# Performance work log

Measured on AMD Instinct MI355X. Metric: run time of the kernel, lower is better.

## Reference

```python
import jax, jax.numpy as jnp
import numpy as np

E = 768
H = 12
D = E // H  # 64


def setup_inputs() -> dict:
    key = jax.random.key(0)
    ks = jax.random.split(key, 12)
    B, S = 4, 2048
    scale = 1.0 / np.sqrt(E)
    inp = {
        "q": jax.random.normal(ks[0], (B, S, E), jnp.float32),
        "k": jax.random.normal(ks[1], (B, S, E), jnp.float32),
        "v": jax.random.normal(ks[2], (B, S, E), jnp.float32),
        "mask": jax.random.randint(ks[3], (B, S), 0, 2, jnp.int32),
        "Wq": jax.random.normal(ks[4], (E, E), jnp.float32) * scale,
        "bq": jnp.zeros((E,), jnp.float32),
        "Wk": jax.random.normal(ks[5], (E, E), jnp.float32) * scale,
        "bk": jnp.zeros((E,), jnp.float32),
        "Wv": jax.random.normal(ks[6], (E, E), jnp.float32) * scale,
        "bv": jnp.zeros((E,), jnp.float32),
        "Wo": jax.random.normal(ks[7], (E, E), jnp.float32) * scale,
        "bo": jnp.zeros((E,), jnp.float32),
    }
    return inp


def reference(q, k, v, mask, Wq, bq, Wk, bk, Wv, bv, Wo, bo):
    B, Sq, _ = q.shape
    Sk = k.shape[1]
    # QKV projections, split into heads: [B, H, S, D]
    qh = (q @ Wq + bq).reshape(B, Sq, H, D).transpose(0, 2, 1, 3)
    kh = (k @ Wk + bk).reshape(B, Sk, H, D).transpose(0, 2, 1, 3)
    vh = (v @ Wv + bv).reshape(B, Sk, H, D).transpose(0, 2, 1, 3)
    scores = jnp.einsum("bhqd,bhkd->bhqk", qh, kh) / jnp.sqrt(jnp.float32(D))
    # enc=True padding-mask path: positions where mask==0 get -1e9 added
    bias = jnp.where(mask == 0, jnp.float32(-1e9), jnp.float32(0.0))  # [B, Sk]
    scores = scores + bias[:, None, None, :]
    weights = jax.nn.softmax(scores, axis=-1)
    # dropout is identity in eval mode
    ctx = jnp.einsum("bhqk,bhkd->bqhd", weights, vh).reshape(B, Sq, E)
    return ctx @ Wo + bo
```

## Files before the change

kernel.cpp:

```cpp
#include <hip/hip_runtime.h>
#include <hip/hip_bf16.h>
#include <stdint.h>


typedef __bf16 bf16x8 __attribute__((ext_vector_type(8)));
typedef __bf16 bf16x4 __attribute__((ext_vector_type(4)));
typedef float floatx4 __attribute__((ext_vector_type(4)));

#define MFMA_BF16(a, b, c) __builtin_amdgcn_mfma_f32_16x16x32_bf16(a, b, c, 0, 0, 0)


__device__ __forceinline__ void glds16(const __bf16* g, __bf16* l) {
  __builtin_amdgcn_global_load_lds(
      (const __attribute__((address_space(1))) unsigned int*)g,
      (__attribute__((address_space(3))) unsigned int*)l, 16, 0, 0);
}

#if __has_builtin(__builtin_amdgcn_permlane32_swap)
__device__ __forceinline__ void perm32_swap(unsigned int& a, unsigned int& b) {
  auto r = __builtin_amdgcn_permlane32_swap(a, b, false, false);
  a = r[0];
  b = r[1];
}
#else
__device__ __forceinline__ void perm32_swap(unsigned int& a, unsigned int& b) {
  asm("v_permlane32_swap_b32 %0, %1" : "+v"(a), "+v"(b));
}
#endif

#if __has_builtin(__builtin_amdgcn_permlane16_swap)
__device__ __forceinline__ void perm16_swap(unsigned int& a, unsigned int& b) {
  auto r = __builtin_amdgcn_permlane16_swap(a, b, false, false);
  a = r[0];
  b = r[1];
}
#else
__device__ __forceinline__ void perm16_swap(unsigned int& a, unsigned int& b) {
  asm("v_permlane16_swap_b32 %0, %1" : "+v"(a), "+v"(b));
}
#endif

__global__ __launch_bounds__(256) void prep_transpose(
    const float* __restrict__ W0, const float* __restrict__ W1,
    const float* __restrict__ W2, const float* __restrict__ W3,
    __bf16* __restrict__ T0, __bf16* __restrict__ T1,
    __bf16* __restrict__ T2, __bf16* __restrict__ T3,
    const int* __restrict__ mask, float* __restrict__ biasF) {
  const int z = blockIdx.z;
  const float* W = (z == 0) ? W0 : (z == 1) ? W1 : (z == 2) ? W2 : W3;
  __bf16* T = (z == 0) ? T0 : (z == 1) ? T1 : (z == 2) ? T2 : T3;
  __shared__ float t[32][33];
  const int tx = threadIdx.x & 31, ty = threadIdx.x >> 5;
  const int kb = blockIdx.x * 32, nb = blockIdx.y * 32;
#pragma unroll
  for (int j = 0; j < 4; ++j)
    t[ty + j * 8][tx] = W[(size_t)(kb + ty + j * 8) * 768 + nb + tx];
  if (z == 3 && blockIdx.y == 0 && blockIdx.x < 8) {
    const int idx = blockIdx.x * 1024 + threadIdx.x * 4;
    const int4 m4 = *(const int4*)&mask[idx];
    float4 f4;
    f4.x = m4.x ? 0.0f : -1e5f;
    f4.y = m4.y ? 0.0f : -1e5f;
    f4.z = m4.z ? 0.0f : -1e5f;
    f4.w = m4.w ? 0.0f : -1e5f;
    *(float4*)&biasF[idx] = f4;
  }
  __syncthreads();
#pragma unroll
  for (int j = 0; j < 4; ++j)
    T[(size_t)(nb + ty + j * 8) * 768 + kb + tx] = (__bf16)t[tx][ty + j * 8];
}

__global__ __launch_bounds__(256) void qkv_gemm(
    const __bf16* __restrict__ Wtq, const __bf16* __restrict__ Wtk,
    const __bf16* __restrict__ Wtv, const float* __restrict__ Xq,
    const float* __restrict__ Xk, const float* __restrict__ Xv,
    const float* __restrict__ bq, const float* __restrict__ bk,
    const float* __restrict__ bv, __bf16* __restrict__ Qh,
    __bf16* __restrict__ Kh, __bf16* __restrict__ Vt) {
  __shared__ __align__(16) __bf16 As[2][128 * 32];
  __shared__ __align__(16) __bf16 Bs[2][128 * 32];
  const int gid = blockIdx.x + 6 * blockIdx.y + 384 * blockIdx.z;
  const int swz = (gid & 7) * 144 + (gid >> 3);
  const int z = swz / 384;
  const int rem = swz - z * 384;
  const int by = rem / 6;
  const int bx = rem - by * 6;

  const __bf16* Aop = (z == 0) ? Wtq : (z == 1) ? Wtk : Wtv;
  const float* Bop = (z == 0) ? Xq : (z == 1) ? Xk : Xv;
  const float* bias = (z == 0) ? bq : (z == 1) ? bk : bv;
  __bf16* Dst = (z == 0) ? Qh : (z == 1) ? Kh : Vt;
  const int m0 = bx * 128, n0 = by * 128;

  const int tid = threadIdx.x, lane = tid & 63, w = tid >> 6;
  const int quad = lane >> 4, l16 = lane & 15;
  const int wm = (w >> 1) * 64, wn = (w & 1) * 64;

  const int garow = w * 32 + (lane >> 2);
  const int gacol = (lane & 3) * 8;
  const __bf16* gA = Aop + (size_t)(m0 + garow) * 768 + gacol;
  const int brow = tid >> 3, bcol = (tid & 7) * 4;
  const float* gB = Bop + (size_t)(n0 + brow) * 768 + bcol;

  floatx4 acc[4][4] = {};
  float4 f[4];

  glds16(gA, &As[0][w * 1024]);
  glds16(gA + (size_t)16 * 768, &As[0][w * 1024 + 512]);
#pragma unroll
  for (int j = 0; j < 4; ++j) f[j] = *(const float4*)&gB[(size_t)(32 * j) * 768];
#pragma unroll
  for (int j = 0; j < 4; ++j) {
    bf16x4 pv;
    pv[0] = (__bf16)f[j].x; pv[1] = (__bf16)f[j].y;
    pv[2] = (__bf16)f[j].z; pv[3] = (__bf16)f[j].w;
    *(bf16x4*)&Bs[0][(brow + 32 * j) * 32 + bcol] = pv;
  }
#pragma unroll
  for (int j = 0; j < 4; ++j) f[j] = *(const float4*)&gB[(size_t)(32 * j) * 768 + 32];
  __syncthreads();

#pragma unroll 2
  for (int it = 0; it < 24; ++it) {
    const int c = it & 1;
    if (it < 23) {
      glds16(gA + (size_t)(it + 1) * 32, &As[c ^ 1][w * 1024]);
      glds16(gA + (size_t)(it + 1) * 32 + (size_t)16 * 768,
             &As[c ^ 1][w * 1024 + 512]);
    }
    bf16x8 af[4], bfr[4];
#pragma unroll
    for (int t = 0; t < 4; ++t) {
      af[t] = *(const bf16x8*)&As[c][(wm + t * 16 + l16) * 32 + quad * 8];
      bfr[t] = *(const bf16x8*)&Bs[c][(wn + t * 16 + l16) * 32 + quad * 8];
    }
    if (it < 23) {
#pragma unroll
      for (int j = 0; j < 4; ++j) {
        bf16x4 pv;
        pv[0] = (__bf16)f[j].x; pv[1] = (__bf16)f[j].y;
        pv[2] = (__bf16)f[j].z; pv[3] = (__bf16)f[j].w;
        *(bf16x4*)&Bs[c ^ 1][(brow + 32 * j) * 32 + bcol] = pv;
      }
    }
    if (it < 22) {
#pragma unroll
      for (int j = 0; j < 4; ++j)
        f[j] = *(const float4*)&gB[(size_t)(32 * j) * 768 + (it + 2) * 32];
    }
#pragma unroll
    for (int mt = 0; mt < 4; ++mt)
#pragma unroll
      for (int nt = 0; nt < 4; ++nt)
        acc[mt][nt] = MFMA_BF16(af[mt], bfr[nt], acc[mt][nt]);
    __syncthreads();
  }

  const float qs = (z == 0) ? 0.18033688011112042f : 1.0f;
#pragma unroll
  for (int mt = 0; mt < 4; ++mt) {
    const int e = m0 + wm + mt * 16 + quad * 4;
    const float4 b4 = *(const float4*)&bias[e];
    const int h = e >> 6, d = e & 63;
#pragma unroll
    for (int nt = 0; nt < 4; ++nt) {
      const int s = n0 + wn + nt * 16 + l16;
      const int bb = s >> 11, sr = s & 2047;
      const float v0 = (acc[mt][nt][0] + b4.x) * qs;
      const float v1 = (acc[mt][nt][1] + b4.y) * qs;
      const float v2 = (acc[mt][nt][2] + b4.z) * qs;
      const float v3 = (acc[mt][nt][3] + b4.w) * qs;
      if (z < 2) {
        bf16x4 pv;
        pv[0] = (__bf16)v0; pv[1] = (__bf16)v1; pv[2] = (__bf16)v2; pv[3] = (__bf16)v3;
        const int col = (z == 0) ? d : ((((d >> 3) ^ (sr & 7)) << 3) | (d & 7));
        *(bf16x4*)&Dst[((size_t)(bb * 12 + h) * 2048 + sr) * 64 + col] = pv;
      } else {
        const size_t rowbase = ((size_t)(bb * 12 + h) * 64 + d) * 2048;
        const int shi = sr & ~63, sblk = (sr >> 3) & 7, soff = sr & 7;
        Dst[rowbase + 0 * 2048 + shi + (((sblk ^ ((d + 0) & 7))) << 3) + soff] = (__bf16)v0;
        Dst[rowbase + 1 * 2048 + shi + (((sblk ^ ((d + 1) & 7))) << 3) + soff] = (__bf16)v1;
        Dst[rowbase + 2 * 2048 + shi + (((sblk ^ ((d + 2) & 7))) << 3) + soff] = (__bf16)v2;
        Dst[rowbase + 3 * 2048 + shi + (((sblk ^ ((d + 3) & 7))) << 3) + soff] = (__bf16)v3;
      }
    }
  }
}

__global__ __launch_bounds__(256) void out_gemm(const __bf16* __restrict__ Wto,
                                                const __bf16* __restrict__ Ctx,
                                                const float* __restrict__ bo,
                                                float* __restrict__ Out) {
  __shared__ __align__(16) __bf16 As[2][128 * 32];
  __shared__ __align__(16) __bf16 Bs[2][128 * 32];
  const int gid = blockIdx.x + 6 * blockIdx.y;
  const int swz = (gid & 7) * 48 + (gid >> 3);
  const int by = swz / 6;
  const int bx = swz - by * 6;
  const int m0 = bx * 128, n0 = by * 128;
  const int tid = threadIdx.x, lane = tid & 63, w = tid >> 6;
  const int quad = lane >> 4, l16 = lane & 15;
  const int wm = (w >> 1) * 64, wn = (w & 1) * 64;

  const int grow = w * 32 + (lane >> 2);
  const int gcol = (lane & 3) * 8;
  const __bf16* gA = Wto + (size_t)(m0 + grow) * 768 + gcol;
  const __bf16* gB = Ctx + (size_t)(n0 + grow) * 768 + gcol;

  floatx4 acc[4][4] = {};

  glds16(gA, &As[0][w * 1024]);
  glds16(gA + (size_t)16 * 768, &As[0][w * 1024 + 512]);
  glds16(gB, &Bs[0][w * 1024]);
  glds16(gB + (size_t)16 * 768, &Bs[0][w * 1024 + 512]);
  __syncthreads();

#pragma unroll 2
  for (int it = 0; it < 24; ++it) {
    const int c = it & 1;
    if (it < 23) {
      glds16(gA + (size_t)(it + 1) * 32, &As[c ^ 1][w * 1024]);
      glds16(gA + (size_t)(it + 1) * 32 + (size_t)16 * 768,
             &As[c ^ 1][w * 1024 + 512]);
      glds16(gB + (size_t)(it + 1) * 32, &Bs[c ^ 1][w * 1024]);
      glds16(gB + (size_t)(it + 1) * 32 + (size_t)16 * 768,
             &Bs[c ^ 1][w * 1024 + 512]);
    }
    bf16x8 af[4], bfr[4];
#pragma unroll
    for (int t = 0; t < 4; ++t) {
      af[t] = *(const bf16x8*)&As[c][(wm + t * 16 + l16) * 32 + quad * 8];
      bfr[t] = *(const bf16x8*)&Bs[c][(wn + t * 16 + l16) * 32 + quad * 8];
    }
#pragma unroll
    for (int mt = 0; mt < 4; ++mt)
#pragma unroll
      for (int nt = 0; nt < 4; ++nt)
        acc[mt][nt] = MFMA_BF16(af[mt], bfr[nt], acc[mt][nt]);
    __syncthreads();
  }

#pragma unroll
  for (int mt = 0; mt < 4; ++mt) {
    const int e = m0 + wm + mt * 16 + quad * 4;
    const float4 b4 = *(const float4*)&bo[e];
#pragma unroll
    for (int nt = 0; nt < 4; ++nt) {
      const int s = n0 + wn + nt * 16 + l16;
      float4 r;
      r.x = acc[mt][nt][0] + b4.x;
      r.y = acc[mt][nt][1] + b4.y;
      r.z = acc[mt][nt][2] + b4.z;
      r.w = acc[mt][nt][3] + b4.w;
      *(float4*)&Out[(size_t)s * 768 + e] = r;
    }
  }
}

__global__ __launch_bounds__(256) void attn_kernel(
    const __bf16* __restrict__ Qh, const __bf16* __restrict__ Kh,
    const __bf16* __restrict__ Vt, const float* __restrict__ biasF,
    __bf16* __restrict__ ctx) {
  const int lid = blockIdx.x + 16 * blockIdx.y;
  const int swz = (lid & 7) * 96 + (lid >> 3);
  const int qx = swz & 15, bh = swz >> 4;
  const int b = bh / 12, h = bh - b * 12;
  const int tid = threadIdx.x, lane = tid & 63, w = tid >> 6;
  const int quad = lane >> 4, l16 = lane & 15;
  const int q0 = qx * 128 + w * 32;

  __shared__ __align__(16) __bf16 Ks[2][64 * 64];
  __shared__ __align__(16) __bf16 Vs[2][64 * 64];

  const __bf16* Qbase = Qh + (size_t)bh * 2048 * 64;
  const __bf16* Kbase = Kh + (size_t)bh * 2048 * 64;
  const __bf16* Vbase = Vt + (size_t)bh * 64 * 2048;
  const float* biasB = biasF + b * 2048;

  bf16x8 bqf[2][2];
#pragma unroll
  for (int qt = 0; qt < 2; ++qt)
#pragma unroll
    for (int c = 0; c < 2; ++c)
      bqf[qt][c] =
          *(const bf16x8*)&Qbase[(size_t)(q0 + qt * 16 + l16) * 64 + c * 32 + quad * 8];

  const int r0 = (w * 2) * 8 + (lane >> 3);
  const int r1 = (w * 2 + 1) * 8 + (lane >> 3);
  const int scol = (lane & 7) * 8;
  const int d0 = (w * 2) * 512;
  const int d1 = (w * 2 + 1) * 512;
  const int col0 = (quad ^ (l16 & 7)) * 8;

  glds16(&Kbase[(size_t)r0 * 64 + scol], &Ks[0][d0]);
  glds16(&Kbase[(size_t)r1 * 64 + scol], &Ks[0][d1]);
  glds16(&Vbase[(size_t)r0 * 2048 + scol], &Vs[0][d0]);
  glds16(&Vbase[(size_t)r1 * 2048 + scol], &Vs[0][d1]);

  floatx4 o[4][2] = {};
  floatx4 os[2] = {};
  bf16x8 ones8;
#pragma unroll
  for (int j = 0; j < 8; ++j) ones8[j] = (__bf16)1.0f;

  for (int it = 0; it < 32; ++it) {
    const int kt = it * 64;
    const int cur = it & 1;
    const int nxt = cur ^ 1;
    const int nkt = (kt + 64) & 2047;

    __syncthreads();

    glds16(&Kbase[(size_t)(nkt + r0) * 64 + scol], &Ks[nxt][d0]);
    glds16(&Kbase[(size_t)(nkt + r1) * 64 + scol], &Ks[nxt][d1]);
    glds16(&Vbase[(size_t)r0 * 2048 + nkt + scol], &Vs[nxt][d0]);
    glds16(&Vbase[(size_t)r1 * 2048 + nkt + scol], &Vs[nxt][d1]);

    floatx4 sc[4][2];
#pragma unroll
    for (int t = 0; t < 4; ++t) {
      const float4 bf4 = *(const float4*)&biasB[kt + t * 16 + quad * 4];
      bf16x8 ak0 = *(const bf16x8*)&Ks[cur][(t * 16 + l16) * 64 + col0];
      bf16x8 ak1 = *(const bf16x8*)&Ks[cur][(t * 16 + l16) * 64 + (col0 ^ 32)];
#pragma unroll
      for (int qt = 0; qt < 2; ++qt) {
        floatx4 zz;
        zz[0] = bf4.x; zz[1] = bf4.y; zz[2] = bf4.z; zz[3] = bf4.w;
        zz = MFMA_BF16(ak0, bqf[qt][0], zz);
        zz = MFMA_BF16(ak1, bqf[qt][1], zz);
        sc[t][qt] = zz;
      }
    }
    unsigned int u[4][2][2];
#pragma unroll
    for (int t = 0; t < 4; ++t)
#pragma unroll
      for (int qt = 0; qt < 2; ++qt) {
        const float e0 = __builtin_amdgcn_exp2f(sc[t][qt][0]);
        const float e1 = __builtin_amdgcn_exp2f(sc[t][qt][1]);
        const float e2 = __builtin_amdgcn_exp2f(sc[t][qt][2]);
        const float e3 = __builtin_amdgcn_exp2f(sc[t][qt][3]);
        asm("v_cvt_pk_bf16_f32 %0, %1, %2" : "=v"(u[t][qt][0]) : "v"(e0), "v"(e1));
        asm("v_cvt_pk_bf16_f32 %0, %1, %2" : "=v"(u[t][qt][1]) : "v"(e2), "v"(e3));
      }
#pragma unroll
    for (int c = 0; c < 2; ++c) {
      bf16x8 bp[2];
#pragma unroll
      for (int qt = 0; qt < 2; ++qt) {
        unsigned int w0 = u[2 * c][qt][0], w1 = u[2 * c][qt][1];
        unsigned int w2 = u[2 * c + 1][qt][0], w3 = u[2 * c + 1][qt][1];
        perm32_swap(w0, w2);
        perm32_swap(w1, w3);
        perm16_swap(w0, w2);
        perm16_swap(w1, w3);
        union { unsigned int wd[4]; bf16x8 v; } ub;
        ub.wd[0] = w0; ub.wd[1] = w1; ub.wd[2] = w2; ub.wd[3] = w3;
        bp[qt] = ub.v;
        os[qt] = MFMA_BF16(ones8, bp[qt], os[qt]);
      }
#pragma unroll
      for (int dt = 0; dt < 4; ++dt) {
        bf16x8 av = *(const bf16x8*)&Vs[cur][(dt * 16 + l16) * 64 + (col0 ^ (c * 32))];
#pragma unroll
        for (int qt = 0; qt < 2; ++qt) o[dt][qt] = MFMA_BF16(av, bp[qt], o[dt][qt]);
      }
    }
  }

  float inv[2];
  inv[0] = 1.0f / os[0][0];
  inv[1] = 1.0f / os[1][0];
#pragma unroll
  for (int dt = 0; dt < 4; ++dt)
#pragma unroll
    for (int qt = 0; qt < 2; ++qt) {
      const int q = q0 + qt * 16 + l16;
      const int d = h * 64 + dt * 16 + quad * 4;
      bf16x4 pv;
      pv[0] = (__bf16)(o[dt][qt][0] * inv[qt]);
      pv[1] = (__bf16)(o[dt][qt][1] * inv[qt]);
      pv[2] = (__bf16)(o[dt][qt][2] * inv[qt]);
      pv[3] = (__bf16)(o[dt][qt][3] * inv[qt]);
      *(bf16x4*)&ctx[(size_t)(b * 2048 + q) * 768 + d] = pv;
    }
}

extern "C" void kernel_launch(void* const* d_in, const int* in_sizes, int n_in,
                              void* d_out, int out_size, void* d_ws, size_t ws_size,
                              hipStream_t stream) {
  const float* q = (const float*)d_in[0];
  const float* k = (const float*)d_in[1];
  const float* v = (const float*)d_in[2];
  const int* mask = (const int*)d_in[3];
  const float* Wq = (const float*)d_in[4];
  const float* bq = (const float*)d_in[5];
  const float* Wk = (const float*)d_in[6];
  const float* bk = (const float*)d_in[7];
  const float* Wv = (const float*)d_in[8];
  const float* bv = (const float*)d_in[9];
  const float* Wo = (const float*)d_in[10];
  const float* bo = (const float*)d_in[11];
  float* out = (float*)d_out;

  char* ws = (char*)d_ws;
  const size_t SZ = (size_t)8192 * 768 * 2;
  const size_t WSZ = (size_t)768 * 768 * 2;
  __bf16* Qh = (__bf16*)(ws);
  __bf16* Kh = (__bf16*)(ws + SZ);
  __bf16* Vt = (__bf16*)(ws + 2 * SZ);
  __bf16* ctx = (__bf16*)(ws + 3 * SZ);
  __bf16* Wtq = (__bf16*)(ws + 4 * SZ);
  __bf16* Wtk = (__bf16*)(ws + 4 * SZ + WSZ);
  __bf16* Wtv = (__bf16*)(ws + 4 * SZ + 2 * WSZ);
  __bf16* Wto = (__bf16*)(ws + 4 * SZ + 3 * WSZ);
  float* biasF = (float*)(ws + 4 * SZ + 4 * WSZ);

  prep_transpose<<<dim3(24, 24, 4), 256, 0, stream>>>(Wq, Wk, Wv, Wo, Wtq, Wtk,
                                                      Wtv, Wto, mask, biasF);
  qkv_gemm<<<dim3(6, 64, 3), 256, 0, stream>>>(Wtq, Wtk, Wtv, q, k, v, bq, bk, bv,
                                               Qh, Kh, Vt);
  attn_kernel<<<dim3(16, 48), 256, 0, stream>>>(Qh, Kh, Vt, biasF, ctx);
  out_gemm<<<dim3(6, 64), 256, 0, stream>>>(Wto, ctx, bo, out);
}
```

Before: 300.5 us.

## Load fp32 activations via direct-to-LDS, swizzle LDS tiles, add MFMA priority hints

The QKV GEMM now stages fp32 activations straight into LDS with async global_load_lds and converts them to bf16 when reading fragments. This replaces the register round-trip and separate bf16 store. Both GEMMs gain an XOR swizzle on LDS columns to reduce bank conflicts, and the barrier moves to the top of the loop. The attention kernel wraps its MFMA sections in s_setprio hints. The cost is doubled LDS footprint for the B tile and conversion work repeated per fragment read.

```diff
diff --git a/kernel.cpp b/kernel.cpp
--- a/kernel.cpp
+++ b/kernel.cpp
@@ -10,7 +10,7 @@
 #define MFMA_BF16(a, b, c) __builtin_amdgcn_mfma_f32_16x16x32_bf16(a, b, c, 0, 0, 0)
 
 
-__device__ __forceinline__ void glds16(const __bf16* g, __bf16* l) {
+__device__ __forceinline__ void glds16(const void* g, void* l) {
   __builtin_amdgcn_global_load_lds(
       (const __attribute__((address_space(1))) unsigned int*)g,
       (__attribute__((address_space(3))) unsigned int*)l, 16, 0, 0);
@@ -79,7 +79,7 @@
     const float* __restrict__ bv, __bf16* __restrict__ Qh,
     __bf16* __restrict__ Kh, __bf16* __restrict__ Vt) {
   __shared__ __align__(16) __bf16 As[2][128 * 32];
-  __shared__ __align__(16) __bf16 Bs[2][128 * 32];
+  __shared__ __align__(16) float Bsf[2][128 * 32];
   const int gid = blockIdx.x + 6 * blockIdx.y + 384 * blockIdx.z;
   const int swz = (gid & 7) * 144 + (gid >> 3);
   const int z = swz / 384;
@@ -98,63 +98,55 @@
   const int wm = (w >> 1) * 64, wn = (w & 1) * 64;
 
   const int garow = w * 32 + (lane >> 2);
-  const int gacol = (lane & 3) * 8;
+  const int gacol = (((lane & 3) ^ ((lane >> 3) & 3)) * 8);
   const __bf16* gA = Aop + (size_t)(m0 + garow) * 768 + gacol;
-  const int brow = tid >> 3, bcol = (tid & 7) * 4;
-  const float* gB = Bop + (size_t)(n0 + brow) * 768 + bcol;
+  const int gbrow = w * 32 + (lane >> 3);
+  const int gbcol = (((lane & 7) ^ ((lane >> 3) & 7)) * 4);
+  const float* gB = Bop + (size_t)(n0 + gbrow) * 768 + gbcol;
+
+  const int colA = (quad ^ ((l16 >> 1) & 3)) * 8;
+  const int blkB = (2 * quad) ^ (l16 & 7);
 
   floatx4 acc[4][4] = {};
-  float4 f[4];
 
   glds16(gA, &As[0][w * 1024]);
   glds16(gA + (size_t)16 * 768, &As[0][w * 1024 + 512]);
 #pragma unroll
-  for (int j = 0; j < 4; ++j) f[j] = *(const float4*)&gB[(size_t)(32 * j) * 768];
-#pragma unroll
-  for (int j = 0; j < 4; ++j) {
-    bf16x4 pv;
-    pv[0] = (__bf16)f[j].x; pv[1] = (__bf16)f[j].y;
-    pv[2] = (__bf16)f[j].z; pv[3] = (__bf16)f[j].w;
-    *(bf16x4*)&Bs[0][(brow + 32 * j) * 32 + bcol] = pv;
-  }
-#pragma unroll
-  for (int j = 0; j < 4; ++j) f[j] = *(const float4*)&gB[(size_t)(32 * j) * 768 + 32];
-  __syncthreads();
+  for (int j = 0; j < 4; ++j)
+    glds16(gB + (size_t)(8 * j) * 768, &Bsf[0][w * 1024 + j * 256]);
 
 #pragma unroll 2
   for (int it = 0; it < 24; ++it) {
     const int c = it & 1;
+    __syncthreads();
     if (it < 23) {
       glds16(gA + (size_t)(it + 1) * 32, &As[c ^ 1][w * 1024]);
       glds16(gA + (size_t)(it + 1) * 32 + (size_t)16 * 768,
              &As[c ^ 1][w * 1024 + 512]);
+#pragma unroll
+      for (int j = 0; j < 4; ++j)
+        glds16(gB + (size_t)(8 * j) * 768 + (it + 1) * 32,
+               &Bsf[c ^ 1][w * 1024 + j * 256]);
     }
     bf16x8 af[4], bfr[4];
 #pragma unroll
     for (int t = 0; t < 4; ++t) {
-      af[t] = *(const bf16x8*)&As[c][(wm + t * 16 + l16) * 32 + quad * 8];
-      bfr[t] = *(const bf16x8*)&Bs[c][(wn + t * 16 + l16) * 32 + quad * 8];
-    }
-    if (it < 23) {
-#pragma unroll
-      for (int j = 0; j < 4; ++j) {
-        bf16x4 pv;
-        pv[0] = (__bf16)f[j].x; pv[1] = (__bf16)f[j].y;
-        pv[2] = (__bf16)f[j].z; pv[3] = (__bf16)f[j].w;
-        *(bf16x4*)&Bs[c ^ 1][(brow + 32 * j) * 32 + bcol] = pv;
-      }
-    }
-    if (it < 22) {
-#pragma unroll
-      for (int j = 0; j < 4; ++j)
-        f[j] = *(const float4*)&gB[(size_t)(32 * j) * 768 + (it + 2) * 32];
+      af[t] = *(const bf16x8*)&As[c][(wm + t * 16 + l16) * 32 + colA];
+      const int r = (wn + t * 16 + l16) * 32;
+      const float4 fa = *(const float4*)&Bsf[c][r + blkB * 4];
+      const float4 fb = *(const float4*)&Bsf[c][r + (blkB ^ 1) * 4];
+      bf16x8 bb;
+      bb[0] = (__bf16)fa.x; bb[1] = (__bf16)fa.y;
+      bb[2] = (__bf16)fa.z; bb[3] = (__bf16)fa.w;
+      bb[4] = (__bf16)fb.x; bb[5] = (__bf16)fb.y;
+      bb[6] = (__bf16)fb.z; bb[7] = (__bf16)fb.w;
+      bfr[t] = bb;
     }
 #pragma unroll
     for (int mt = 0; mt < 4; ++mt)
 #pragma unroll
       for (int nt = 0; nt < 4; ++nt)
         acc[mt][nt] = MFMA_BF16(af[mt], bfr[nt], acc[mt][nt]);
-    __syncthreads();
   }
 
   const float qs = (z == 0) ? 0.18033688011112042f : 1.0f;
@@ -204,9 +196,10 @@
   const int wm = (w >> 1) * 64, wn = (w & 1) * 64;
 
   const int grow = w * 32 + (lane >> 2);
-  const int gcol = (lane & 3) * 8;
+  const int gcol = (((lane & 3) ^ ((lane >> 3) & 3)) * 8);
   const __bf16* gA = Wto + (size_t)(m0 + grow) * 768 + gcol;
   const __bf16* gB = Ctx + (size_t)(n0 + grow) * 768 + gcol;
+  const int colA = (quad ^ ((l16 >> 1) & 3)) * 8;
 
   floatx4 acc[4][4] = {};
 
@@ -214,11 +207,11 @@
   glds16(gA + (size_t)16 * 768, &As[0][w * 1024 + 512]);
   glds16(gB, &Bs[0][w * 1024]);
   glds16(gB + (size_t)16 * 768, &Bs[0][w * 1024 + 512]);
-  __syncthreads();
 
 #pragma unroll 2
   for (int it = 0; it < 24; ++it) {
     const int c = it & 1;
+    __syncthreads();
     if (it < 23) {
       glds16(gA + (size_t)(it + 1) * 32, &As[c ^ 1][w * 1024]);
       glds16(gA + (size_t)(it + 1) * 32 + (size_t)16 * 768,
@@ -230,15 +223,14 @@
     bf16x8 af[4], bfr[4];
 #pragma unroll
     for (int t = 0; t < 4; ++t) {
-      af[t] = *(const bf16x8*)&As[c][(wm + t * 16 + l16) * 32 + quad * 8];
-      bfr[t] = *(const bf16x8*)&Bs[c][(wn + t * 16 + l16) * 32 + quad * 8];
+      af[t] = *(const bf16x8*)&As[c][(wm + t * 16 + l16) * 32 + colA];
+      bfr[t] = *(const bf16x8*)&Bs[c][(wn + t * 16 + l16) * 32 + colA];
     }
 #pragma unroll
     for (int mt = 0; mt < 4; ++mt)
 #pragma unroll
       for (int nt = 0; nt < 4; ++nt)
         acc[mt][nt] = MFMA_BF16(af[mt], bfr[nt], acc[mt][nt]);
-    __syncthreads();
   }
 
 #pragma unroll
@@ -318,6 +310,7 @@
     glds16(&Vbase[(size_t)r1 * 2048 + nkt + scol], &Vs[nxt][d1]);
 
     floatx4 sc[4][2];
+    __builtin_amdgcn_s_setprio(1);
 #pragma unroll
     for (int t = 0; t < 4; ++t) {
       const float4 bf4 = *(const float4*)&biasB[kt + t * 16 + quad * 4];
@@ -332,6 +325,7 @@
         sc[t][qt] = zz;
       }
     }
+    __builtin_amdgcn_s_setprio(0);
     unsigned int u[4][2][2];
 #pragma unroll
     for (int t = 0; t < 4; ++t)
@@ -358,14 +352,17 @@
         union { unsigned int wd[4]; bf16x8 v; } ub;
         ub.wd[0] = w0; ub.wd[1] = w1; ub.wd[2] = w2; ub.wd[3] = w3;
         bp[qt] = ub.v;
-        os[qt] = MFMA_BF16(ones8, bp[qt], os[qt]);
       }
+      __builtin_amdgcn_s_setprio(1);
+      os[0] = MFMA_BF16(ones8, bp[0], os[0]);
+      os[1] = MFMA_BF16(ones8, bp[1], os[1]);
 #pragma unroll
       for (int dt = 0; dt < 4; ++dt) {
         bf16x8 av = *(const bf16x8*)&Vs[cur][(dt * 16 + l16) * 64 + (col0 ^ (c * 32))];
 #pragma unroll
         for (int qt = 0; qt < 2; ++qt) o[dt][qt] = MFMA_BF16(av, bp[qt], o[dt][qt]);
       }
+      __builtin_amdgcn_s_setprio(0);
     }
   }
 
```

New measurement: 331.1 us. +10.2%, slower.
